# Performance work log

Measured on AMD Instinct MI355X. Metric: run time of the kernel, lower is better.

## Reference

```python
import jax, jax.numpy as jnp
import numpy as np

N = 131072

def setup_inputs() -> dict:
    key = jax.random.key(0)
    k_x, k_e, k_w2, k_b2, k_w3, k_b3, k_w4 = jax.random.split(key, 7)
    x = jax.random.randint(k_x, (N, 32), 0, 7424, dtype=jnp.int32)
    emb = jax.random.normal(k_e, (7424, 128), dtype=jnp.float32) * 0.05
    W2 = jax.random.normal(k_w2, (32, 128), dtype=jnp.float32) * 0.05
    b2 = jax.random.normal(k_b2, (32,), dtype=jnp.float32) * 0.05
    W3 = jax.random.normal(k_w3, (32, 64), dtype=jnp.float32) * 0.05
    b3 = jax.random.normal(k_b3, (32,), dtype=jnp.float32) * 0.05
    W4 = jax.random.normal(k_w4, (1, 64), dtype=jnp.float32) * 0.05
    return {"x": x, "emb": emb, "W2": W2, "b2": b2, "W3": W3, "b3": b3, "W4": W4}

def reference(x, emb, W2, b2, W3, b3, W4):
    # x: [N, 32] int indices; use first 29 slots
    idx = x[..., :29]
    h = emb[idx].sum(axis=-2)                    # [N, 128] embedding-bag sum
    h = jax.nn.relu(h)
    h = h @ W2.T + b2                            # [N, 32]
    h = jax.nn.relu(jnp.concatenate((h, -h), axis=-1))   # [N, 64] sign-concat
    h = h @ W3.T + b3                            # [N, 32]
    h = jax.nn.relu(jnp.concatenate((h, -h), axis=-1))   # [N, 64]
    return h @ W4.T                              # [N, 1] (no bias)
```

## Files before the change

kernel.cpp:

```cpp
#include <hip/hip_runtime.h>
#include <hip/hip_fp16.h>


typedef _Float16 h2v_t  __attribute__((ext_vector_type(2)));
typedef _Float16 half8  __attribute__((ext_vector_type(8)));
typedef float    f32x4  __attribute__((ext_vector_type(4)));

constexpr int RPB = 64;

__global__ __launch_bounds__(256) void emb_to_fp16(
    const float* __restrict__ emb, __half2* __restrict__ emb16,
    int npairs_real, int npairs_tot)
{
    int i = blockIdx.x * blockDim.x + threadIdx.x;
    if (i < npairs_tot) {
        float2 v = make_float2(0.f, 0.f);
        if (i < npairs_real) v = ((const float2*)emb)[i];
        emb16[i] = __floats2half2_rn(v.x, v.y);
    }
}

__global__ __launch_bounds__(256) void w_to_fp16(
    const float* __restrict__ W2, const float* __restrict__ W3,
    _Float16* __restrict__ W2h, _Float16* __restrict__ W3h)
{
    int i = blockIdx.x * blockDim.x + threadIdx.x;
    if (i < 4096) W2h[i] = (_Float16)W2[i];
    if (i < 2048) W3h[i] = (_Float16)W3[i];
}

__global__ __launch_bounds__(256, 6) void nnue_one(
    const int*      __restrict__ x,
    const __half*   __restrict__ emb16,
    const _Float16* __restrict__ W2h,
    const _Float16* __restrict__ W3h,
    const float*    __restrict__ b2,
    const float*    __restrict__ b3,
    const float*    __restrict__ W4,
    float*          __restrict__ out, int n)
{
    __shared__ uint4 hT[4][16 * 17];
    __shared__ __align__(16) char scratch[4][2176];

    const int tid  = threadIdx.x;
    const int lane = tid & 63;
    const int wave = tid >> 6;
    const int row0 = blockIdx.x * RPB;
    const int wrow0 = __builtin_amdgcn_readfirstlane(row0 + wave * 16);

    const int g   = lane >> 4;
    const int sub = lane & 15;
    const unsigned subOff = (unsigned)sub * 16u;

    int* xw = (int*)&scratch[wave][0];

    {
        const int4* xb = (const int4*)(x + (size_t)wrow0 * 32);
        int4 a = xb[lane * 2];
        int4 b = xb[lane * 2 + 1];
        if ((lane & 3) == 3) { b.y = 7424; b.z = 7424; b.w = 7424; }
        ((int4*)xw)[lane * 2]     = a;
        ((int4*)xw)[lane * 2 + 1] = b;
    }

    #pragma unroll 4
    for (int r = 0; r < 16; ++r) {
        const int* xrow = &xw[r * 32 + g];
        uint4 v[8];
        #pragma unroll
        for (int b = 0; b < 8; ++b) {
            const int idx = xrow[4 * b];
            const unsigned off = ((unsigned)idx << 8) + subOff;
            v[b] = *(const uint4*)((const char*)emb16 + off);
        }
        h2v_t hacc[4];
        #pragma unroll
        for (int q = 0; q < 4; ++q) hacc[q] = (h2v_t)0;
        #pragma unroll
        for (int b = 0; b < 8; ++b) {
            hacc[0] += __builtin_bit_cast(h2v_t, v[b].x);
            hacc[1] += __builtin_bit_cast(h2v_t, v[b].y);
            hacc[2] += __builtin_bit_cast(h2v_t, v[b].z);
            hacc[3] += __builtin_bit_cast(h2v_t, v[b].w);
        }
        #pragma unroll
        for (int q = 0; q < 4; ++q) {
            unsigned u = __builtin_bit_cast(unsigned, hacc[q]);
            h2v_t t = __builtin_bit_cast(h2v_t, u);
            t += __builtin_bit_cast(h2v_t, (unsigned)__shfl_xor((int)u, 16));
            unsigned u2 = __builtin_bit_cast(unsigned, t);
            t += __builtin_bit_cast(h2v_t, (unsigned)__shfl_xor((int)u2, 32));
            hacc[q] = __builtin_elementwise_max(t, (h2v_t)0);
        }
        if (g == 0) {
            uint4 o;
            o.x = __builtin_bit_cast(unsigned, hacc[0]);
            o.y = __builtin_bit_cast(unsigned, hacc[1]);
            o.z = __builtin_bit_cast(unsigned, hacc[2]);
            o.w = __builtin_bit_cast(unsigned, hacc[3]);
            hT[wave][r * 17 + sub] = o;
        }
    }

    const int q  = lane >> 4;
    const int nn = lane & 15;

    half8 bw2[2][4];
    #pragma unroll
    for (int nt = 0; nt < 2; ++nt)
        #pragma unroll
        for (int kk = 0; kk < 4; ++kk)
            bw2[nt][kk] = __builtin_bit_cast(half8,
                *(const uint4*)((const char*)W2h +
                    ((nt * 16 + nn) * 128 + kk * 32 + q * 8) * 2));

    half8 af[4];
    #pragma unroll
    for (int kk = 0; kk < 4; ++kk)
        af[kk] = __builtin_bit_cast(half8, hT[wave][nn * 17 + (4 * kk + q)]);

    f32x4 acc0 = {0.f, 0.f, 0.f, 0.f}, acc1 = {0.f, 0.f, 0.f, 0.f};
    #pragma unroll
    for (int kk = 0; kk < 4; ++kk) {
        acc0 = __builtin_amdgcn_mfma_f32_16x16x32_f16(af[kk], bw2[0][kk], acc0, 0, 0, 0);
        acc1 = __builtin_amdgcn_mfma_f32_16x16x32_f16(af[kk], bw2[1][kk], acc1, 0, 0, 0);
    }
    const float bb0 = b2[nn], bb1 = b2[16 + nn];

    _Float16* a2 = (_Float16*)&scratch[wave][0];
    #pragma unroll
    for (int r = 0; r < 4; ++r) {
        const float v0 = acc0[r] + bb0;
        const float v1 = acc1[r] + bb1;
        const int m = q * 4 + r;
        a2[m * 68 + nn]      = (_Float16)fmaxf(v0, 0.f);
        a2[m * 68 + 16 + nn] = (_Float16)fmaxf(v1, 0.f);
        a2[m * 68 + 32 + nn] = (_Float16)fmaxf(-v0, 0.f);
        a2[m * 68 + 48 + nn] = (_Float16)fmaxf(-v1, 0.f);
    }

    half8 bw3[2][2];
    #pragma unroll
    for (int nt = 0; nt < 2; ++nt)
        #pragma unroll
        for (int kk = 0; kk < 2; ++kk)
            bw3[nt][kk] = __builtin_bit_cast(half8,
                *(const uint4*)((const char*)W3h +
                    ((nt * 16 + nn) * 64 + kk * 32 + q * 8) * 2));

    half8 a2f[2];
    #pragma unroll
    for (int kk = 0; kk < 2; ++kk) {
        const _Float16* p = &a2[nn * 68 + kk * 32 + q * 8];
        half8 t;
        #pragma unroll
        for (int j = 0; j < 8; ++j) t[j] = p[j];
        a2f[kk] = t;
    }

    f32x4 acc30 = {0.f, 0.f, 0.f, 0.f}, acc31 = {0.f, 0.f, 0.f, 0.f};
    #pragma unroll
    for (int kk = 0; kk < 2; ++kk) {
        acc30 = __builtin_amdgcn_mfma_f32_16x16x32_f16(a2f[kk], bw3[0][kk], acc30, 0, 0, 0);
        acc31 = __builtin_amdgcn_mfma_f32_16x16x32_f16(a2f[kk], bw3[1][kk], acc31, 0, 0, 0);
    }
    const float bb30 = b3[nn], bb31 = b3[16 + nn];

    const float w4a = W4[nn],      w4b = W4[16 + nn];
    const float w4c = W4[32 + nn], w4d = W4[48 + nn];
    float o[4];
    #pragma unroll
    for (int r = 0; r < 4; ++r) {
        const float v0 = acc30[r] + bb30;
        const float v1 = acc31[r] + bb31;
        o[r] = fmaxf(v0, 0.f) * w4a + fmaxf(-v0, 0.f) * w4c
             + fmaxf(v1, 0.f) * w4b + fmaxf(-v1, 0.f) * w4d;
    }
    #pragma unroll
    for (int s = 1; s < 16; s <<= 1) {
        #pragma unroll
        for (int r = 0; r < 4; ++r) o[r] += __shfl_xor(o[r], s);
    }
    if (nn == 0) {
        #pragma unroll
        for (int r = 0; r < 4; ++r) {
            const int row = wrow0 + q * 4 + r;
            if (row < n) out[row] = o[r];
        }
    }
}

__global__ __launch_bounds__(256) void nnue_fused(
    const int*    __restrict__ x,
    const __half* __restrict__ emb16,
    const float*  __restrict__ W2, const float* __restrict__ b2,
    const float*  __restrict__ W3, const float* __restrict__ b3,
    const float*  __restrict__ W4,
    float*        __restrict__ out, int n)
{
    __shared__ int     xlds[4][512];
    __shared__ __half2 hbuf[64][65];
    __shared__ float   h2T[32 * 64];
    __shared__ float   obuf[4][64];

    const int tid  = threadIdx.x;
    const int lane = tid & 63;
    const int wave = tid >> 6;
    const int row0 = blockIdx.x * RPB;
    const int wrow0 = __builtin_amdgcn_readfirstlane(row0 + wave * 16);
    const int g   = lane >> 4;
    const int sub = lane & 15;
    const unsigned subOff = (unsigned)sub * 16u;

    {
        const int4* xb = (const int4*)(x + (size_t)wrow0 * 32);
        int4 a = xb[lane * 2];
        int4 b = xb[lane * 2 + 1];
        if ((lane & 3) == 3) { b.y = 7424; b.z = 7424; b.w = 7424; }
        ((int4*)&xlds[wave][0])[lane * 2]     = a;
        ((int4*)&xlds[wave][0])[lane * 2 + 1] = b;
    }

    #pragma unroll 4
    for (int r = 0; r < 16; ++r) {
        const int* xrow = &xlds[wave][r * 32 + g];
        uint4 v[8];
        #pragma unroll
        for (int b = 0; b < 8; ++b) {
            const int idx = xrow[4 * b];
            const unsigned off = ((unsigned)idx << 8) + subOff;
            v[b] = *(const uint4*)((const char*)emb16 + off);
        }
        h2v_t hacc[4];
        #pragma unroll
        for (int q = 0; q < 4; ++q) hacc[q] = (h2v_t)0;
        #pragma unroll
        for (int b = 0; b < 8; ++b) {
            hacc[0] += __builtin_bit_cast(h2v_t, v[b].x);
            hacc[1] += __builtin_bit_cast(h2v_t, v[b].y);
            hacc[2] += __builtin_bit_cast(h2v_t, v[b].z);
            hacc[3] += __builtin_bit_cast(h2v_t, v[b].w);
        }
        #pragma unroll
        for (int q = 0; q < 4; ++q) {
            unsigned u = __builtin_bit_cast(unsigned, hacc[q]);
            h2v_t t = __builtin_bit_cast(h2v_t, u);
            t += __builtin_bit_cast(h2v_t, (unsigned)__shfl_xor((int)u, 16));
            unsigned u2 = __builtin_bit_cast(unsigned, t);
            t += __builtin_bit_cast(h2v_t, (unsigned)__shfl_xor((int)u2, 32));
            hacc[q] = __builtin_elementwise_max(t, (h2v_t)0);
        }
        if (g == 0) {
            const int row = wave * 16 + r;
            #pragma unroll
            for (int q = 0; q < 4; ++q)
                hbuf[row][sub * 4 + q] = __builtin_bit_cast(__half2, hacc[q]);
        }
    }
    __syncthreads();

    {
        const int j0 = wave * 8;
        const int rr = lane;
        float acc[8];
        #pragma unroll
        for (int j = 0; j < 8; ++j) acc[j] = b2[j0 + j];
        #pragma unroll
        for (int d2 = 0; d2 < 64; ++d2) {
            const __half2 hv = hbuf[rr][d2];
            const float vx = __low2float(hv), vy = __high2float(hv);
            #pragma unroll
            for (int j = 0; j < 8; ++j) {
                const float* w = W2 + (size_t)(j0 + j) * 128 + d2 * 2;
                acc[j] = fmaf(vx, w[0], acc[j]);
                acc[j] = fmaf(vy, w[1], acc[j]);
            }
        }
        #pragma unroll
        for (int j = 0; j < 8; ++j) h2T[(j0 + j) * 64 + rr] = acc[j];
    }
    __syncthreads();

    {
        const int j0 = wave * 8;
        const int rr = lane;
        float h2v[32];
        #pragma unroll
        for (int k = 0; k < 32; ++k) h2v[k] = h2T[k * 64 + rr];
        float acc[8];
        #pragma unroll
        for (int j = 0; j < 8; ++j) acc[j] = b3[j0 + j];
        #pragma unroll
        for (int k = 0; k < 32; ++k) {
            const float p = fmaxf(h2v[k], 0.f);
            const float m = fmaxf(-h2v[k], 0.f);
            #pragma unroll
            for (int j = 0; j < 8; ++j) {
                const float* w = W3 + (size_t)(j0 + j) * 64;
                acc[j] = fmaf(p, w[k],      acc[j]);
                acc[j] = fmaf(m, w[32 + k], acc[j]);
            }
        }
        float o = 0.f;
        #pragma unroll
        for (int j = 0; j < 8; ++j) {
            const int jj = j0 + j;
            o = fmaf(fmaxf(acc[j], 0.f),  W4[jj],      o);
            o = fmaf(fmaxf(-acc[j], 0.f), W4[32 + jj], o);
        }
        obuf[wave][rr] = o;
    }
    __syncthreads();

    if (tid < 64) {
        const int row = row0 + tid;
        if (row < n)
            out[row] = obuf[0][tid] + obuf[1][tid] + obuf[2][tid] + obuf[3][tid];
    }
}

extern "C" void kernel_launch(void* const* d_in, const int* in_sizes, int n_in,
                              void* d_out, int out_size, void* d_ws, size_t ws_size,
                              hipStream_t stream) {
    const int*   x   = (const int*)  d_in[0];
    const float* emb = (const float*)d_in[1];
    const float* W2  = (const float*)d_in[2];
    const float* b2  = (const float*)d_in[3];
    const float* W3  = (const float*)d_in[4];
    const float* b3  = (const float*)d_in[5];
    const float* W4  = (const float*)d_in[6];
    float* out = (float*)d_out;
    const int n = out_size;

    __half2* emb16 = (__half2*)d_ws;
    const int npairs_real = 7424 * 64;
    const int npairs_tot  = 7425 * 64;
    hipLaunchKernelGGL(emb_to_fp16, dim3((npairs_tot + 255) / 256), dim3(256),
                       0, stream, emb, emb16, npairs_real, npairs_tot);

    const size_t emb_bytes = (size_t)7425 * 256;
    const size_t w2h_off   = emb_bytes;
    const size_t w3h_off   = w2h_off + 8192;
    const size_t need      = w3h_off + 4096;
    const bool   fused_ok  = ws_size >= need;

    if (fused_ok) {
        _Float16* W2h = (_Float16*)((char*)d_ws + w2h_off);
        _Float16* W3h = (_Float16*)((char*)d_ws + w3h_off);
        hipLaunchKernelGGL(w_to_fp16, dim3(16), dim3(256), 0, stream,
                           W2, W3, W2h, W3h);
        hipLaunchKernelGGL(nnue_one, dim3((n + RPB - 1) / RPB), dim3(256),
                           0, stream, x, (const __half*)emb16, W2h, W3h,
                           b2, b3, W4, out, n);
    } else {
        hipLaunchKernelGGL(nnue_fused, dim3((n + RPB - 1) / RPB), dim3(256),
                           0, stream, x, (const __half*)emb16, W2, b2, W3, b3,
                           W4, out, n);
    }
}
```

Before: 121.6 us.

## Skip padded gathers, pack indices to 16-bit LDS, merge prep kernels

Each row's 29 indices are now gathered with 7 loads per lane plus one extra load on the first lane group only. This drops the three wasted gathers of the zero padding row that the old 8-load loop issued. Indices are packed to 16 bits in LDS, the layer-2 activation scratch reuses the hT buffer, and launch bounds move from 6 to 7 waves to cut LDS and allow more occupancy. The two fp16 conversion kernels are merged into one launch, which now writes W2h/W3h even when the workspace is too small for them.

```diff
diff --git a/kernel.cpp b/kernel.cpp
--- a/kernel.cpp
+++ b/kernel.cpp
@@ -8,9 +8,11 @@
 
 constexpr int RPB = 64;
 
-__global__ __launch_bounds__(256) void emb_to_fp16(
-    const float* __restrict__ emb, __half2* __restrict__ emb16,
-    int npairs_real, int npairs_tot)
+__global__ __launch_bounds__(256) void prep_fp16(
+    const float* __restrict__ emb, const float* __restrict__ W2,
+    const float* __restrict__ W3,
+    __half2* __restrict__ emb16, _Float16* __restrict__ W2h,
+    _Float16* __restrict__ W3h, int npairs_real, int npairs_tot)
 {
     int i = blockIdx.x * blockDim.x + threadIdx.x;
     if (i < npairs_tot) {
@@ -18,18 +20,11 @@
         if (i < npairs_real) v = ((const float2*)emb)[i];
         emb16[i] = __floats2half2_rn(v.x, v.y);
     }
-}
-
-__global__ __launch_bounds__(256) void w_to_fp16(
-    const float* __restrict__ W2, const float* __restrict__ W3,
-    _Float16* __restrict__ W2h, _Float16* __restrict__ W3h)
-{
-    int i = blockIdx.x * blockDim.x + threadIdx.x;
     if (i < 4096) W2h[i] = (_Float16)W2[i];
     if (i < 2048) W3h[i] = (_Float16)W3[i];
 }
 
-__global__ __launch_bounds__(256, 6) void nnue_one(
+__global__ __launch_bounds__(256, 7) void nnue_one(
     const int*      __restrict__ x,
     const __half*   __restrict__ emb16,
     const _Float16* __restrict__ W2h,
@@ -40,7 +35,7 @@
     float*          __restrict__ out, int n)
 {
     __shared__ uint4 hT[4][16 * 17];
-    __shared__ __align__(16) char scratch[4][2176];
+    __shared__ uint4 xs[4][64];
 
     const int tid  = threadIdx.x;
     const int lane = tid & 63;
@@ -52,32 +47,42 @@
     const int sub = lane & 15;
     const unsigned subOff = (unsigned)sub * 16u;
 
-    int* xw = (int*)&scratch[wave][0];
-
     {
         const int4* xb = (const int4*)(x + (size_t)wrow0 * 32);
         int4 a = xb[lane * 2];
         int4 b = xb[lane * 2 + 1];
-        if ((lane & 3) == 3) { b.y = 7424; b.z = 7424; b.w = 7424; }
-        ((int4*)xw)[lane * 2]     = a;
-        ((int4*)xw)[lane * 2 + 1] = b;
+        uint4 p;
+        p.x = (unsigned)(a.x & 0xffff) | ((unsigned)a.y << 16);
+        p.y = (unsigned)(a.z & 0xffff) | ((unsigned)a.w << 16);
+        p.z = (unsigned)(b.x & 0xffff) | ((unsigned)b.y << 16);
+        p.w = (unsigned)(b.z & 0xffff) | ((unsigned)b.w << 16);
+        xs[wave][lane] = p;
     }
 
     #pragma unroll 4
     for (int r = 0; r < 16; ++r) {
-        const int* xrow = &xw[r * 32 + g];
-        uint4 v[8];
-        #pragma unroll
-        for (int b = 0; b < 8; ++b) {
-            const int idx = xrow[4 * b];
+        const unsigned short* xrow = (const unsigned short*)&xs[wave][0] + r * 32;
+
+        uint4 v[7];
+        #pragma unroll
+        for (int b = 0; b < 7; ++b) {
+            const int idx = xrow[4 * b + g];
             const unsigned off = ((unsigned)idx << 8) + subOff;
             v[b] = *(const uint4*)((const char*)emb16 + off);
         }
+        uint4 v7 = make_uint4(0u, 0u, 0u, 0u);
+        if (g == 0) {
+            const int idx28 = xrow[28];
+            v7 = *(const uint4*)((const char*)emb16 +
+                                 (((unsigned)idx28) << 8) + subOff);
+        }
+
         h2v_t hacc[4];
         #pragma unroll
-        for (int q = 0; q < 4; ++q) hacc[q] = (h2v_t)0;
-        #pragma unroll
-        for (int b = 0; b < 8; ++b) {
+        for (int q = 0; q < 4; ++q)
+            hacc[q] = __builtin_bit_cast(h2v_t, (&v7.x)[q]);
+        #pragma unroll
+        for (int b = 0; b < 7; ++b) {
             hacc[0] += __builtin_bit_cast(h2v_t, v[b].x);
             hacc[1] += __builtin_bit_cast(h2v_t, v[b].y);
             hacc[2] += __builtin_bit_cast(h2v_t, v[b].z);
@@ -127,7 +132,9 @@
     }
     const float bb0 = b2[nn], bb1 = b2[16 + nn];
 
-    _Float16* a2 = (_Float16*)&scratch[wave][0];
+    asm volatile("" ::: "memory");
+
+    _Float16* a2 = (_Float16*)&hT[wave][0];
     #pragma unroll
     for (int r = 0; r < 4; ++r) {
         const float v0 = acc0[r] + bb0;
@@ -138,6 +145,7 @@
         a2[m * 68 + 32 + nn] = (_Float16)fmaxf(-v0, 0.f);
         a2[m * 68 + 48 + nn] = (_Float16)fmaxf(-v1, 0.f);
     }
+    asm volatile("" ::: "memory");
 
     half8 bw3[2][2];
     #pragma unroll
@@ -332,23 +340,23 @@
     float* out = (float*)d_out;
     const int n = out_size;
 
-    __half2* emb16 = (__half2*)d_ws;
-    const int npairs_real = 7424 * 64;
-    const int npairs_tot  = 7425 * 64;
-    hipLaunchKernelGGL(emb_to_fp16, dim3((npairs_tot + 255) / 256), dim3(256),
-                       0, stream, emb, emb16, npairs_real, npairs_tot);
-
     const size_t emb_bytes = (size_t)7425 * 256;
     const size_t w2h_off   = emb_bytes;
     const size_t w3h_off   = w2h_off + 8192;
     const size_t need      = w3h_off + 4096;
     const bool   fused_ok  = ws_size >= need;
 
+    __half2*  emb16 = (__half2*)d_ws;
+    _Float16* W2h   = (_Float16*)((char*)d_ws + w2h_off);
+    _Float16* W3h   = (_Float16*)((char*)d_ws + w3h_off);
+    const int npairs_real = 7424 * 64;
+    const int npairs_tot  = 7425 * 64;
+
+    hipLaunchKernelGGL(prep_fp16, dim3((npairs_tot + 255) / 256), dim3(256),
+                       0, stream, emb, W2, W3, emb16, W2h, W3h,
+                       npairs_real, npairs_tot);
+
     if (fused_ok) {
-        _Float16* W2h = (_Float16*)((char*)d_ws + w2h_off);
-        _Float16* W3h = (_Float16*)((char*)d_ws + w3h_off);
-        hipLaunchKernelGGL(w_to_fp16, dim3(16), dim3(256), 0, stream,
-                           W2, W3, W2h, W3h);
         hipLaunchKernelGGL(nnue_one, dim3((n + RPB - 1) / RPB), dim3(256),
                            0, stream, x, (const __half*)emb16, W2h, W3h,
                            b2, b3, W4, out, n);
```

Measured after the change: 124.1 us. +2.1%, slower.
